# Performance work log

Measured on AMD Instinct MI355X. Metric: run time of the kernel, lower is better.

Reference implementation:

```python
import jax, jax.numpy as jnp
import numpy as np

N = 1536           # candidates (== pre_nms_k, so pre-selection branch is identity)
H = W = 224        # mask resolution
NCLS = 80
SIGMA = 0.5
POST_NMS_K = 768
SCORE_THRESHOLD = 0.5
EPS = 1e-6


def setup_inputs() -> dict:
    key = jax.random.key(0)
    k1, k2, k3, k4, k5 = jax.random.split(key, 5)
    binary_masks = (jax.random.uniform(k1, (N, H, W)) > 0.5).astype(jnp.float32)
    seg_preds = jax.random.uniform(k2, (N, H, W), dtype=jnp.float32)
    scores = jax.random.uniform(k3, (N,), dtype=jnp.float32)
    cls_labels = jax.random.randint(k4, (N,), 0, NCLS, dtype=jnp.int32)
    cls_factors = jax.random.normal(k5, (N,), dtype=jnp.float32)
    mask_sum = binary_masks.reshape(N, -1).sum(axis=1)  # per-instance area
    return {
        "cls_labels": cls_labels,
        "scores": scores,
        "cls_factors": cls_factors,
        "seg_preds": seg_preds,
        "binary_masks": binary_masks,
        "mask_sum": mask_sum,
    }


def reference(cls_labels, scores, cls_factors, seg_preds, binary_masks, mask_sum):
    """Matrix NMS (SOLOv2) over binary masks; faithful to the torch source.

    Returns fixed-shape, zero-padded (seg_preds, scores, cls_labels, cls_factors)
    with POST_NMS_K rows; padding rows have score 0 / label -1.
    """
    n = scores.shape[0]  # == pre_nms_k, so the torch top-k pre-filter is a no-op
    flat = binary_masks.reshape(n, -1)                    # [N, H*W]
    intersection = flat @ flat.T                          # [N, N] pairwise overlap
    # NOTE: faithful to source: mask_sum.view(1,-1) + mask_sum.view(1,-1)
    # (i.e. 2 * area_j broadcast over rows), reproducing the original's math.
    mask_sum_tile = mask_sum[None, :] + mask_sum[None, :]
    union = mask_sum_tile - intersection
    iou = intersection / (union + EPS)
    iou = jnp.triu(iou, 1)
    labels_match = jnp.triu(
        (cls_labels[None, :] == cls_labels[:, None]).astype(iou.dtype), 1)
    decay_iou = iou * labels_match                        # [N, N]
    compensate_iou = decay_iou.max(axis=0)                # [N]
    comp_mat = compensate_iou[:, None]                    # expand(N,N).T of source
    # gaussian mode
    decay_coefficient = jnp.exp(-(decay_iou ** 2 - comp_mat ** 2) / SIGMA).min(axis=0)
    decayed_scores = scores * decay_coefficient
    valid = decayed_scores >= SCORE_THRESHOLD
    # torch code keeps ORIGINAL scores of surviving rows, then takes top post_nms_k
    sort_key = jnp.where(valid, scores, -1.0)
    _, idx = jax.lax.top_k(sort_key, POST_NMS_K)
    kept_valid = valid[idx]
    out_scores = jnp.where(kept_valid, scores[idx], 0.0)
    out_seg = jnp.where(kept_valid[:, None, None], seg_preds[idx], 0.0)
    out_labels = jnp.where(kept_valid, cls_labels[idx], -1)
    out_factors = jnp.where(kept_valid, cls_factors[idx], 0.0)
    return out_seg, out_scores, out_labels, out_factors
```

## Files before the change

### kernel.cpp

```cpp
#include <hip/hip_runtime.h>
#include <stdint.h>

typedef unsigned long long u64;
typedef unsigned int u32;
typedef unsigned short u16;

#define N_MASKS 1536
#define HW 50176
#define WORDS 784
#define NCLS 80
#define POST_NMS_K 768
#define SEG_ELEMS ((size_t)POST_NMS_K * HW)
#define KEYPAD 2048

#define MMAX 96
#define MAXPAIRS (MMAX*(MMAX-1)/2)
#define TW 112
#define TWP 113
#define NTILES (WORDS/TW)
#define CT 512

__global__ __launch_bounds__(256) void pack_kernel(const float4* __restrict__ masks,
                                                   u64* __restrict__ bits) {
    int gid = blockIdx.x * blockDim.x + threadIdx.x;
    int wave = gid >> 6;
    int lane = gid & 63;
    float4 v[4];
#pragma unroll
    for (int g = 0; g < 4; ++g)
        v[g] = masks[(size_t)wave * 256 + g * 64 + lane];
    u64 w[16];
#pragma unroll
    for (int g = 0; g < 4; ++g) {
        w[g * 4 + 0] = __ballot(v[g].x > 0.5f);
        w[g * 4 + 1] = __ballot(v[g].y > 0.5f);
        w[g * 4 + 2] = __ballot(v[g].z > 0.5f);
        w[g * 4 + 3] = __ballot(v[g].w > 0.5f);
    }
    if (lane < 4) {
#pragma unroll
        for (int g = 0; g < 4; ++g)
            bits[(size_t)wave * 16 + g * 4 + lane] = w[g * 4 + lane];
    }
}

__global__ __launch_bounds__(CT) void classnms_kernel(
        const int* __restrict__ labels, const float* __restrict__ scores,
        const float* __restrict__ msum, const u64* __restrict__ bits,
        float* __restrict__ keys) {
    const int cls = blockIdx.x;
    const int tid = threadIdx.x;
    __shared__ int mem[MMAX];
    __shared__ float Sm[MMAX], Sc[MMAX];
    __shared__ u32 compS[MMAX], Ms[MMAX];
    __shared__ u16 lutAB[MAXPAIRS];
    __shared__ u32 Ipair[MAXPAIRS];
    __shared__ u64 rows[MMAX * TWP];
    __shared__ int scan[CT];
    __shared__ int mtot;

    const int PER = N_MASKS / CT;
    int lab[PER]; int cnt = 0;
#pragma unroll
    for (int k = 0; k < PER; ++k) { lab[k] = labels[tid * PER + k]; cnt += (lab[k] == cls); }
    scan[tid] = cnt;
    __syncthreads();
    for (int off = 1; off < CT; off <<= 1) {
        int vv = scan[tid];
        int uu = (tid >= off) ? scan[tid - off] : 0;
        __syncthreads();
        scan[tid] = vv + uu;
        __syncthreads();
    }
    {
        int o = scan[tid] - cnt;
#pragma unroll
        for (int k = 0; k < PER; ++k)
            if (lab[k] == cls) mem[o++] = tid * PER + k;
    }
    if (tid == CT - 1) mtot = scan[CT - 1];
    __syncthreads();
    const int m = mtot;
    const int np = m * (m - 1) / 2;

    for (int b = tid; b < m; b += CT) {
        int g = mem[b];
        Sm[b] = msum[g]; Sc[b] = scores[g];
        compS[b] = 0u; Ms[b] = 0u;
    }
    for (int p = tid; p < np; p += CT) {
        int bb = (int)((1.0 + sqrt(1.0 + 8.0 * (double)p)) * 0.5);
        while (bb * (bb - 1) / 2 > p) --bb;
        while ((bb + 1) * bb / 2 <= p) ++bb;
        int aa = p - bb * (bb - 1) / 2;
        lutAB[p] = (u16)((aa << 8) | bb);
        Ipair[p] = 0u;
    }

    const int nb = m * (TW / 2);
    for (int t = 0; t < NTILES; ++t) {
        __syncthreads();
        for (int base = 0; base < nb; base += 4 * CT) {
            ulonglong2 vv[4]; int dst[4]; bool ok[4];
#pragma unroll
            for (int u = 0; u < 4; ++u) {
                int blk = base + u * CT + tid;
                ok[u] = (blk < nb);
                if (ok[u]) {
                    int r = blk / (TW / 2), k = blk - r * (TW / 2);
                    dst[u] = r * TWP + 2 * k;
                    vv[u] = *(const ulonglong2*)(bits + (size_t)mem[r] * WORDS
                                                 + t * TW + 2 * k);
                }
            }
#pragma unroll
            for (int u = 0; u < 4; ++u)
                if (ok[u]) { rows[dst[u]] = vv[u].x; rows[dst[u] + 1] = vv[u].y; }
        }
        __syncthreads();
        for (int p = tid; p < np; p += CT) {
            int ab = lutAB[p];
            const u64* ra = &rows[(ab >> 8) * TWP];
            const u64* rb = &rows[(ab & 255) * TWP];
            u32 s = 0;
#pragma unroll 8
            for (int w = 0; w < TW; ++w) s += (u32)__popcll(ra[w] & rb[w]);
            Ipair[p] += s;
        }
    }
    __syncthreads();

    for (int p = tid; p < np; p += CT) {
        int ab = lutAB[p]; int bcol = ab & 255;
        float fI = (float)Ipair[p];
        float D = fI / (2.0f * Sm[bcol] - fI + 1e-6f);
        Ipair[p] = __float_as_uint(D);
        atomicMax(&compS[bcol], __float_as_uint(D));
    }
    __syncthreads();
    for (int p = tid; p < np; p += CT) {
        int ab = lutAB[p]; int aa = ab >> 8; int bcol = ab & 255;
        float D = __uint_as_float(Ipair[p]);
        float ca = __uint_as_float(compS[aa]);
        float v = fmaxf(D * D - ca * ca, 0.0f);
        atomicMax(&Ms[bcol], __float_as_uint(v));
    }
    __syncthreads();
    for (int b = tid; b < m; b += CT) {
        float sc = Sc[b];
        float key = (sc * __expf(-2.0f * __uint_as_float(Ms[b])) >= 0.5f) ? sc : -1.0f;
        keys[mem[b]] = key;
    }
}

__global__ __launch_bounds__(1024) void sortk_kernel(
        const float* __restrict__ keys, const float* __restrict__ scores,
        const int* __restrict__ labels, const float* __restrict__ factors,
        int* __restrict__ sel, float* __restrict__ out_small) {
    __shared__ u64 k2[KEYPAD];
    const int tid = threadIdx.x;
    for (int i = tid; i < KEYPAD; i += 1024) {
        u64 v = 0;
        if (i < N_MASKS) {
            u32 fb = __float_as_uint(keys[i]);
            u32 od = (fb & 0x80000000u) ? ~fb : (fb | 0x80000000u);
            v = ((u64)od << 32) | (u32)(~(u32)i);
        }
        k2[i] = v;
    }
    __syncthreads();
    for (int k = 2; k <= KEYPAD; k <<= 1) {
        for (int j = k >> 1; j > 0; j >>= 1) {
            for (int i = tid; i < KEYPAD; i += 1024) {
                int p = i ^ j;
                if (p > i) {
                    bool desc = ((i & k) == 0);
                    u64 x = k2[i], y = k2[p];
                    if ((x < y) == desc) { k2[i] = y; k2[p] = x; }
                }
            }
            __syncthreads();
        }
    }
    for (int r = tid; r < POST_NMS_K; r += 1024) {
        u64 v = k2[r];
        u32 od = (u32)(v >> 32);
        bool kept = (od >= 0x80000000u);
        int idx = (int)(~(u32)v);
        if (kept) {
            sel[r] = idx;
            out_small[r] = scores[idx];
            out_small[POST_NMS_K + r] = (float)labels[idx];
            out_small[2 * POST_NMS_K + r] = factors[idx];
        } else {
            sel[r] = -1;
            out_small[r] = 0.0f;
            out_small[POST_NMS_K + r] = -1.0f;
            out_small[2 * POST_NMS_K + r] = 0.0f;
        }
    }
}

__global__ __launch_bounds__(256) void gather_kernel(const float4* __restrict__ seg,
                                                     const int* __restrict__ sel,
                                                     float4* __restrict__ out) {
    const int row = blockIdx.y;
    const int s = sel[row];
    const size_t ob = (size_t)row * (HW / 4);
    const size_t ib = (s >= 0) ? (size_t)s * (HW / 4) : 0;
    const float4 z = make_float4(0.f, 0.f, 0.f, 0.f);
#pragma unroll
    for (int u = 0; u < 4; ++u) {
        int col = blockIdx.x * 1024 + u * 256 + threadIdx.x;
        if (col < HW / 4)
            out[ob + col] = (s >= 0) ? seg[ib + col] : z;
    }
}

extern "C" void kernel_launch(void* const* d_in, const int* in_sizes, int n_in,
                              void* d_out, int out_size, void* d_ws, size_t ws_size,
                              hipStream_t stream) {
    const int* labels = (const int*)d_in[0];
    const float* scores = (const float*)d_in[1];
    const float* factors = (const float*)d_in[2];
    const float* seg = (const float*)d_in[3];
    const float* masks = (const float*)d_in[4];
    const float* msum = (const float*)d_in[5];

    float* out = (float*)d_out;
    u64* bits = (u64*)d_out;

    float* keys = (float*)d_ws;
    int* sel = (int*)(keys + N_MASKS);

    {
        int waves = N_MASKS * (HW / 1024);
        pack_kernel<<<waves / 4, 256, 0, stream>>>((const float4*)masks, bits);
    }
    classnms_kernel<<<NCLS, CT, 0, stream>>>(labels, scores, msum, bits, keys);
    sortk_kernel<<<1, 1024, 0, stream>>>(keys, scores, labels, factors, sel,
                                         out + SEG_ELEMS);
    {
        dim3 grid(13, POST_NMS_K);
        gather_kernel<<<grid, 256, 0, stream>>>((const float4*)seg, sel,
                                                (float4*)out);
    }
}
```

Before: 199.6 us.

## Split per-class IoU across blocks, move decay into sort kernel, shuffle-based bitonic

The per-class NMS kernel is split into three blocks per class, each owning an interleaved subset of columns. Each block writes its pairwise IoU values and column maxima to scratch space in the output buffer. The decay reduction and key computation move into the single-block sort kernel. That sort now uses wave shuffles for bitonic stages with stride below 64, and the pack kernel writes one coalesced word per lane. The split raises parallelism from 80 blocks to 240, but each block reloads the same mask bits, and the single sort block now does serial per-element label counting and decay loops.

```diff
diff --git a/kernel.cpp b/kernel.cpp
--- a/kernel.cpp
+++ b/kernel.cpp
@@ -12,52 +12,66 @@
 #define POST_NMS_K 768
 #define SEG_ELEMS ((size_t)POST_NMS_K * HW)
 #define KEYPAD 2048
+#define BITS_BYTES ((size_t)N_MASKS * WORDS * 8)
+#define DP_BYTES ((size_t)NCLS * 4560 * 4)
 
 #define MMAX 96
 #define MAXPAIRS (MMAX*(MMAX-1)/2)
 #define TW 112
 #define TWP 113
+#define TW2 (TW/2)
 #define NTILES (WORDS/TW)
 #define CT 512
+#define KSPLIT 3
+#define PMAX ((MAXPAIRS + KSPLIT - 1)/KSPLIT)
+#define NOWN (MMAX/KSPLIT + 2)
 
 __global__ __launch_bounds__(256) void pack_kernel(const float4* __restrict__ masks,
                                                    u64* __restrict__ bits) {
-    int gid = blockIdx.x * blockDim.x + threadIdx.x;
+    int gid = blockIdx.x * 256 + threadIdx.x;
     int wave = gid >> 6;
     int lane = gid & 63;
-    float4 v[4];
-#pragma unroll
-    for (int g = 0; g < 4; ++g)
-        v[g] = masks[(size_t)wave * 256 + g * 64 + lane];
-    u64 w[16];
-#pragma unroll
-    for (int g = 0; g < 4; ++g) {
-        w[g * 4 + 0] = __ballot(v[g].x > 0.5f);
-        w[g * 4 + 1] = __ballot(v[g].y > 0.5f);
-        w[g * 4 + 2] = __ballot(v[g].z > 0.5f);
-        w[g * 4 + 3] = __ballot(v[g].w > 0.5f);
-    }
-    if (lane < 4) {
-#pragma unroll
-        for (int g = 0; g < 4; ++g)
-            bits[(size_t)wave * 16 + g * 4 + lane] = w[g * 4 + lane];
-    }
-}
-
-__global__ __launch_bounds__(CT) void classnms_kernel(
-        const int* __restrict__ labels, const float* __restrict__ scores,
-        const float* __restrict__ msum, const u64* __restrict__ bits,
-        float* __restrict__ keys) {
-    const int cls = blockIdx.x;
+    const float4* base = masks + (size_t)wave * 1024;
+    u64 keep = 0;
+#pragma unroll
+    for (int h = 0; h < 2; ++h) {
+        float4 v[8];
+#pragma unroll
+        for (int g = 0; g < 8; ++g)
+            v[g] = base[(h * 8 + g) * 64 + lane];
+#pragma unroll
+        for (int g = 0; g < 8; ++g) {
+            int gg = h * 8 + g;
+            u64 b0 = __ballot(v[g].x > 0.5f);
+            u64 b1 = __ballot(v[g].y > 0.5f);
+            u64 b2 = __ballot(v[g].z > 0.5f);
+            u64 b3 = __ballot(v[g].w > 0.5f);
+            keep = (lane == 4 * gg + 0) ? b0 : keep;
+            keep = (lane == 4 * gg + 1) ? b1 : keep;
+            keep = (lane == 4 * gg + 2) ? b2 : keep;
+            keep = (lane == 4 * gg + 3) ? b3 : keep;
+        }
+    }
+    bits[(size_t)wave * 64 + lane] = keep;
+}
+
+__global__ __launch_bounds__(CT) void classd_kernel(
+        const int* __restrict__ labels, const float* __restrict__ msum,
+        const u64* __restrict__ bits, float* __restrict__ Dp,
+        float* __restrict__ compS) {
+    const int cls = blockIdx.x / KSPLIT;
+    const int chunk = blockIdx.x % KSPLIT;
     const int tid = threadIdx.x;
+    __shared__ u64 rows[MMAX * TWP];
     __shared__ int mem[MMAX];
-    __shared__ float Sm[MMAX], Sc[MMAX];
-    __shared__ u32 compS[MMAX], Ms[MMAX];
-    __shared__ u16 lutAB[MAXPAIRS];
-    __shared__ u32 Ipair[MAXPAIRS];
-    __shared__ u64 rows[MMAX * TWP];
+    __shared__ float SmS[MMAX];
+    __shared__ u16 lutA[PMAX], lutB[PMAX];
+    __shared__ u32 Iacc[PMAX];
+    __shared__ u32 colMax[MMAX];
     __shared__ int scan[CT];
-    __shared__ int mtot;
+    __shared__ int ownedOff[NOWN];
+    __shared__ u16 ownedB[NOWN];
+    __shared__ int mtot, Ptot, nOwn;
 
     const int PER = N_MASKS / CT;
     int lab[PER]; int cnt = 0;
@@ -81,23 +95,29 @@
     if (tid == CT - 1) mtot = scan[CT - 1];
     __syncthreads();
     const int m = mtot;
-    const int np = m * (m - 1) / 2;
 
     for (int b = tid; b < m; b += CT) {
-        int g = mem[b];
-        Sm[b] = msum[g]; Sc[b] = scores[g];
-        compS[b] = 0u; Ms[b] = 0u;
-    }
-    for (int p = tid; p < np; p += CT) {
-        int bb = (int)((1.0 + sqrt(1.0 + 8.0 * (double)p)) * 0.5);
-        while (bb * (bb - 1) / 2 > p) --bb;
-        while ((bb + 1) * bb / 2 <= p) ++bb;
-        int aa = p - bb * (bb - 1) / 2;
-        lutAB[p] = (u16)((aa << 8) | bb);
-        Ipair[p] = 0u;
-    }
-
-    const int nb = m * (TW / 2);
+        SmS[b] = msum[mem[b]];
+        colMax[b] = 0u;
+    }
+    if (tid == 0) {
+        int off = 0, j = 0;
+        for (int b = chunk; b < m; b += KSPLIT) {
+            ownedB[j] = (u16)b; ownedOff[j] = off; off += b; ++j;
+        }
+        ownedOff[j] = off; Ptot = off; nOwn = j;
+    }
+    __syncthreads();
+    const int P = Ptot;
+    for (int s = tid; s < P; s += CT) {
+        int j = 0;
+        while (ownedOff[j + 1] <= s) ++j;
+        lutB[s] = ownedB[j];
+        lutA[s] = (u16)(s - ownedOff[j]);
+        Iacc[s] = 0u;
+    }
+
+    const int nb = m * TW2;
     for (int t = 0; t < NTILES; ++t) {
         __syncthreads();
         for (int base = 0; base < nb; base += 4 * CT) {
@@ -107,7 +127,7 @@
                 int blk = base + u * CT + tid;
                 ok[u] = (blk < nb);
                 if (ok[u]) {
-                    int r = blk / (TW / 2), k = blk - r * (TW / 2);
+                    int r = blk / TW2, k = blk - r * TW2;
                     dst[u] = r * TWP + 2 * k;
                     vv[u] = *(const ulonglong2*)(bits + (size_t)mem[r] * WORDS
                                                  + t * TW + 2 * k);
@@ -118,59 +138,88 @@
                 if (ok[u]) { rows[dst[u]] = vv[u].x; rows[dst[u] + 1] = vv[u].y; }
         }
         __syncthreads();
-        for (int p = tid; p < np; p += CT) {
-            int ab = lutAB[p];
-            const u64* ra = &rows[(ab >> 8) * TWP];
-            const u64* rb = &rows[(ab & 255) * TWP];
-            u32 s = 0;
+        for (int s = tid; s < P; s += CT) {
+            const u64* ra = &rows[lutA[s] * TWP];
+            const u64* rb = &rows[lutB[s] * TWP];
+            u32 acc = 0;
 #pragma unroll 8
-            for (int w = 0; w < TW; ++w) s += (u32)__popcll(ra[w] & rb[w]);
-            Ipair[p] += s;
-        }
-    }
-    __syncthreads();
-
-    for (int p = tid; p < np; p += CT) {
-        int ab = lutAB[p]; int bcol = ab & 255;
-        float fI = (float)Ipair[p];
-        float D = fI / (2.0f * Sm[bcol] - fI + 1e-6f);
-        Ipair[p] = __float_as_uint(D);
-        atomicMax(&compS[bcol], __float_as_uint(D));
-    }
-    __syncthreads();
-    for (int p = tid; p < np; p += CT) {
-        int ab = lutAB[p]; int aa = ab >> 8; int bcol = ab & 255;
-        float D = __uint_as_float(Ipair[p]);
-        float ca = __uint_as_float(compS[aa]);
-        float v = fmaxf(D * D - ca * ca, 0.0f);
-        atomicMax(&Ms[bcol], __float_as_uint(v));
-    }
-    __syncthreads();
-    for (int b = tid; b < m; b += CT) {
-        float sc = Sc[b];
-        float key = (sc * __expf(-2.0f * __uint_as_float(Ms[b])) >= 0.5f) ? sc : -1.0f;
-        keys[mem[b]] = key;
-    }
-}
-
-__global__ __launch_bounds__(1024) void sortk_kernel(
-        const float* __restrict__ keys, const float* __restrict__ scores,
-        const int* __restrict__ labels, const float* __restrict__ factors,
+            for (int w = 0; w < TW; ++w) acc += (u32)__popcll(ra[w] & rb[w]);
+            Iacc[s] += acc;
+        }
+    }
+    __syncthreads();
+
+    for (int s = tid; s < P; s += CT) {
+        int bcol = lutB[s];
+        float fI = (float)Iacc[s];
+        float D = fI / (2.0f * SmS[bcol] - fI + 1e-6f);
+        Dp[(size_t)cls * MAXPAIRS + bcol * (bcol - 1) / 2 + lutA[s]] = D;
+        atomicMax(&colMax[bcol], __float_as_uint(D));
+    }
+    __syncthreads();
+    for (int j = tid; j < nOwn; j += CT) {
+        int b = ownedB[j];
+        compS[cls * MMAX + b] = __uint_as_float(colMax[b]);
+    }
+}
+
+__device__ __forceinline__ u64 cmpx(u64 x, int j, bool desc, int lane) {
+    u64 y = __shfl_xor(x, j);
+    bool keepMax = (((lane & j) == 0) == desc);
+    u64 mx = x > y ? x : y, mn = x > y ? y : x;
+    return keepMax ? mx : mn;
+}
+
+__global__ __launch_bounds__(1024) void sortM_kernel(
+        const int* __restrict__ labels, const float* __restrict__ Dp,
+        const float* __restrict__ compS, const float* __restrict__ scores,
+        const float* __restrict__ factors,
         int* __restrict__ sel, float* __restrict__ out_small) {
     __shared__ u64 k2[KEYPAD];
+    __shared__ int lab[N_MASKS];
     const int tid = threadIdx.x;
+    const int lane = tid & 63;
+    const int wv = tid >> 6;
+    for (int i = tid; i < N_MASKS; i += 1024) lab[i] = labels[i];
+    __syncthreads();
     for (int i = tid; i < KEYPAD; i += 1024) {
         u64 v = 0;
         if (i < N_MASKS) {
-            u32 fb = __float_as_uint(keys[i]);
+            int c = lab[i];
+            int b = 0;
+            for (int j = 0; j < i; ++j) b += (lab[j] == c);
+            const float* dp = Dp + (size_t)c * MAXPAIRS + b * (b - 1) / 2;
+            const float* cp = compS + c * MMAX;
+            float M = 0.0f;
+            for (int a = 0; a < b; ++a) {
+                float D = dp[a];
+                float ca = cp[a];
+                M = fmaxf(M, D * D - ca * ca);
+            }
+            float sc = scores[i];
+            float key = (sc * __expf(-2.0f * M) >= 0.5f) ? sc : -1.0f;
+            u32 fb = __float_as_uint(key);
             u32 od = (fb & 0x80000000u) ? ~fb : (fb | 0x80000000u);
             v = ((u64)od << 32) | (u32)(~(u32)i);
         }
         k2[i] = v;
     }
     __syncthreads();
-    for (int k = 2; k <= KEYPAD; k <<= 1) {
-        for (int j = k >> 1; j > 0; j >>= 1) {
+    for (int g = wv; g < KEYPAD / 64; g += 16) {
+        int i = g * 64 + lane;
+        u64 x = k2[i];
+#pragma unroll
+        for (int k = 2; k <= 64; k <<= 1) {
+            bool desc = ((i & k) == 0);
+#pragma unroll
+            for (int j = k >> 1; j >= 1; j >>= 1)
+                x = cmpx(x, j, desc, lane);
+        }
+        k2[i] = x;
+    }
+    __syncthreads();
+    for (int k = 128; k <= KEYPAD; k <<= 1) {
+        for (int j = k >> 1; j >= 64; j >>= 1) {
             for (int i = tid; i < KEYPAD; i += 1024) {
                 int p = i ^ j;
                 if (p > i) {
@@ -181,6 +230,16 @@
             }
             __syncthreads();
         }
+        for (int g = wv; g < KEYPAD / 64; g += 16) {
+            int i = g * 64 + lane;
+            u64 x = k2[i];
+            bool desc = ((i & k) == 0);
+#pragma unroll
+            for (int j = 32; j >= 1; j >>= 1)
+                x = cmpx(x, j, desc, lane);
+            k2[i] = x;
+        }
+        __syncthreads();
     }
     for (int r = tid; r < POST_NMS_K; r += 1024) {
         u64 v = k2[r];
@@ -190,7 +249,7 @@
         if (kept) {
             sel[r] = idx;
             out_small[r] = scores[idx];
-            out_small[POST_NMS_K + r] = (float)labels[idx];
+            out_small[POST_NMS_K + r] = (float)lab[idx];
             out_small[2 * POST_NMS_K + r] = factors[idx];
         } else {
             sel[r] = -1;
@@ -229,17 +288,17 @@
 
     float* out = (float*)d_out;
     u64* bits = (u64*)d_out;
-
-    float* keys = (float*)d_ws;
-    int* sel = (int*)(keys + N_MASKS);
+    float* Dp = (float*)((char*)d_out + BITS_BYTES);
+    float* compS = (float*)((char*)d_out + BITS_BYTES + DP_BYTES);
+
+    int* sel = (int*)d_ws;
 
     {
-        int waves = N_MASKS * (HW / 1024);
-        pack_kernel<<<waves / 4, 256, 0, stream>>>((const float4*)masks, bits);
-    }
-    classnms_kernel<<<NCLS, CT, 0, stream>>>(labels, scores, msum, bits, keys);
-    sortk_kernel<<<1, 1024, 0, stream>>>(keys, scores, labels, factors, sel,
-                                         out + SEG_ELEMS);
+        pack_kernel<<<4704, 256, 0, stream>>>((const float4*)masks, bits);
+    }
+    classd_kernel<<<NCLS * KSPLIT, CT, 0, stream>>>(labels, msum, bits, Dp, compS);
+    sortM_kernel<<<1, 1024, 0, stream>>>(labels, Dp, compS, scores, factors,
+                                         sel, out + SEG_ELEMS);
     {
         dim3 grid(13, POST_NMS_K);
         gather_kernel<<<grid, 256, 0, stream>>>((const float4*)seg, sel,
```

New measurement: 250.0 us. 25.3% more time.
